# Kernel optimization log

Measured on AMD Instinct MI355X. Metric: run time of the kernel, lower is better.

Reference implementation:

```python
import jax, jax.numpy as jnp
import numpy as np

B, D, E, H = 8192, 512, 16, 128  # batch, input_dim, num_experts, hidden_dim
EPS = 1e-5  # BatchNorm eps (torch default)


def setup_inputs() -> dict:
    key = jax.random.key(0)
    ks = iter(jax.random.split(key, 32))
    def n(shape, s=0.05):
        return jax.random.normal(next(ks), shape, dtype=jnp.float32) * s
    inp = {"x": jax.random.normal(next(ks), (B, D), dtype=jnp.float32)}
    # Router params, stacked over the 2 branches (gender, race)
    inp["rbn_gamma"] = jnp.ones((2, D), jnp.float32)
    inp["rbn_beta"] = jnp.zeros((2, D), jnp.float32)
    inp["rbn_mean"] = n((2, D))
    inp["rbn_var"] = jnp.ones((2, D), jnp.float32)
    inp["rW1"], inp["rb1"] = n((2, D, 64)), jnp.full((2, 64), 0.1, jnp.float32)
    inp["rW2"], inp["rb2"] = n((2, 64, 32)), jnp.full((2, 32), 0.1, jnp.float32)
    inp["rW3"], inp["rb3"] = n((2, 32, E)), jnp.full((2, E), 0.1, jnp.float32)
    # Expert params, stacked over [branch=2, expert=16]
    inp["ebn_gamma"] = jnp.ones((2, E, D), jnp.float32)
    inp["ebn_beta"] = jnp.zeros((2, E, D), jnp.float32)
    inp["ebn_mean"] = n((2, E, D))
    inp["ebn_var"] = jnp.ones((2, E, D), jnp.float32)
    inp["eW1"], inp["eb1"] = n((2, E, D, H)), jnp.full((2, E, H), 0.1, jnp.float32)
    inp["eW2"], inp["eb2"] = n((2, E, H, H // 2)), jnp.full((2, E, H // 2), 0.1, jnp.float32)
    inp["eW3"], inp["eb3"] = n((2, E, H // 2)), jnp.full((2, E), 0.1, jnp.float32)
    inp["branch_weights"] = jnp.array([0.5, 0.5], jnp.float32)
    return inp


def reference(x, rbn_gamma, rbn_beta, rbn_mean, rbn_var, rW1, rb1, rW2, rb2,
              rW3, rb3, ebn_gamma, ebn_beta, ebn_mean, ebn_var, eW1, eb1,
              eW2, eb2, eW3, eb3, branch_weights):
    def branch(c):
        # Router: BN(eval) -> Linear(64) -> ReLU -> Linear(32) -> ReLU -> Linear(E) -> Softmax
        xn = (x - rbn_mean[c]) * jax.lax.rsqrt(rbn_var[c] + EPS) * rbn_gamma[c] + rbn_beta[c]
        h = jax.nn.relu(xn @ rW1[c] + rb1[c])
        h = jax.nn.relu(h @ rW2[c] + rb2[c])
        rw = jax.nn.softmax(h @ rW3[c] + rb3[c], axis=1)  # [B, E]
        # Experts batched over E: per-expert BN(eval) -> Linear -> ReLU -> Linear -> ReLU -> Linear -> sigmoid
        m, v = ebn_mean[c][:, None, :], ebn_var[c][:, None, :]
        g, b = ebn_gamma[c][:, None, :], ebn_beta[c][:, None, :]
        xe = (x[None] - m) * jax.lax.rsqrt(v + EPS) * g + b          # [E, B, D]
        h1 = jax.nn.relu(jnp.einsum('ebd,edh->ebh', xe, eW1[c]) + eb1[c][:, None, :])
        h2 = jax.nn.relu(jnp.einsum('ebh,ehk->ebk', h1, eW2[c]) + eb2[c][:, None, :])
        out = jax.nn.sigmoid(jnp.einsum('ebk,ek->eb', h2, eW3[c]) + eb3[c][:, None])  # [E, B]
        return jnp.einsum('be,eb->b', rw, out)                        # weighted sum over experts
    gender_pred = branch(0)
    race_pred = branch(1)
    return branch_weights[0] * gender_pred + branch_weights[1] * race_pred
```

## Files before the change

kernel.cpp:

```cpp
#include <hip/hip_runtime.h>

typedef __attribute__((ext_vector_type(8))) short short8;
typedef __attribute__((ext_vector_type(8))) unsigned short ushort8;
typedef __attribute__((ext_vector_type(4))) float f32x4;
typedef unsigned int u32;
typedef unsigned short u16;

#define AS_GLOBAL(p) ((const __attribute__((address_space(1))) u32*)(p))
#define AS_LDS(p) ((__attribute__((address_space(3))) u32*)(p))

#define NB 8192
#define ND 512
#define NH 128

#define OFF_XPK    0u
#define OFF_W1PK   8388608u
#define OFF_W2PK   12582912u
#define OFF_RW1PT  13107200u
#define OFF_B1P    13238272u
#define OFF_RB1P   13254656u
#define OFF_RWT    13255168u
#define OFF_PBIAS  14303744u

__device__ __forceinline__ u16 f2bf(float f) {
  union { float f; u32 u; } v; v.f = f;
  return (u16)((v.u + 0x7FFFu + ((v.u >> 16) & 1u)) >> 16);
}

__global__ __launch_bounds__(256) void k_prep_all(
    const float* __restrict__ x, u16* __restrict__ xpk,
    const float* __restrict__ eg, const float* __restrict__ ebb,
    const float* __restrict__ em, const float* __restrict__ ev,
    const float* __restrict__ eW1, u16* __restrict__ w1pk, float* __restrict__ pbias,
    const float* __restrict__ eW2, u16* __restrict__ w2pk,
    const float* __restrict__ rbn_g, const float* __restrict__ rbn_b,
    const float* __restrict__ rbn_m, const float* __restrict__ rbn_v,
    const float* __restrict__ rW1, const float* __restrict__ rb1,
    u16* __restrict__ rw1pt, float* __restrict__ rb1p,
    float* __restrict__ out)
{
  __shared__ __align__(16) unsigned char sh[17920];
  const int blk = blockIdx.x, t = threadIdx.x;
  if (blk < 2048) {
    int i = (blk * 256 + t) * 8;
    const float4* p = (const float4*)(x + i);
    float4 v0 = p[0], v1 = p[1];
    ushort8 r;
    r[0] = f2bf(v0.x); r[1] = f2bf(v0.y); r[2] = f2bf(v0.z); r[3] = f2bf(v0.w);
    r[4] = f2bf(v1.x); r[5] = f2bf(v1.y); r[6] = f2bf(v1.z); r[7] = f2bf(v1.w);
    int row = i >> 9, k0 = i & 511;
    int rb = row >> 4, lr = row & 15, kb = k0 >> 5, q = (k0 >> 3) & 3;
    *(ushort8*)(xpk + ((u32)(rb * 16 + kb) * 64 + q * 16 + lr) * 8) = r;
  } else if (blk < 2304) {
    float* sa = (float*)sh;
    float* sc = sa + 64;
    u16* tile = (u16*)(sc + 64);
    float* pb2 = (float*)(tile + 64 * 128);
    const int pair = (blk - 2048) >> 3, dc = (blk - 2048) & 7;
    const int d0 = dc * 64;
    if (t < 64) {
      int d = pair * ND + d0 + t;
      float a = eg[d] * rsqrtf(ev[d] + 1e-5f);
      sa[t] = a;
      sc[t] = ebb[d] - em[d] * a;
    }
    __syncthreads();
    const int h = t & 127, pr = t >> 7;
    float acc = 0.f;
    const float* src = eW1 + (size_t)pair * ND * NH + (size_t)d0 * NH;
#pragma unroll
    for (int i = 0; i < 32; ++i) {
      int dl = i * 2 + pr;
      float w = src[dl * NH + h];
      tile[dl * 128 + h] = f2bf(w * sa[dl]);
      acc += w * sc[dl];
    }
    pb2[pr * 128 + h] = acc;
    __syncthreads();
    {
      int hh = t >> 1, half = t & 1;
      const int nb = hh >> 4, lr = hh & 15;
#pragma unroll
      for (int v8 = 0; v8 < 4; ++v8) {
        int db = d0 + half * 32 + v8 * 8;
        int kb = db >> 5, q = (db >> 3) & 3;
        ushort8 r;
#pragma unroll
        for (int j = 0; j < 8; ++j) r[j] = tile[(half * 32 + v8 * 8 + j) * 128 + hh];
        *(ushort8*)(w1pk + (u32)((pair * 16 + kb) * 8 + nb) * 512 + (q * 16 + lr) * 8) = r;
      }
    }
    if (t < 128) pbias[(u32)(pair * 8 + dc) * 128 + t] = pb2[t] + pb2[128 + t];
  } else if (blk < 2336) {
    const int pair = blk - 2304;
    const float* w2 = eW2 + (size_t)pair * NH * 64;
    int n = t & 63, kk = t >> 6;
    for (int k = kk * 32; k < kk * 32 + 32; ++k) {
      u32 dst = ((u32)((pair * 4 + (k >> 5)) * 4 + (n >> 4))) * 512
              + (((k >> 3) & 3) * 16 + (n & 15)) * 8 + (k & 7);
      w2pk[dst] = f2bf(w2[k * 64 + n]);
    }
  } else if (blk < 2338) {
    const int c = blk - 2336;
    int n = t >> 2, q = t & 3;
    const float* g  = rbn_g + c * ND;
    const float* b  = rbn_b + c * ND;
    const float* m  = rbn_m + c * ND;
    const float* vv = rbn_v + c * ND;
    const float* w1 = rW1 + (size_t)c * ND * 64;
    float acc = 0.f;
    for (int d = q * 128; d < q * 128 + 128; ++d) {
      float a  = g[d] * rsqrtf(vv[d] + 1e-5f);
      float cc = b[d] - m[d] * a;
      float w  = w1[d * 64 + n];
      rw1pt[((u32)c * 64 + n) * ND + d] = f2bf(a * w);
      acc += cc * w;
    }
    acc += __shfl_xor(acc, 1, 64);
    acc += __shfl_xor(acc, 2, 64);
    if (q == 0) rb1p[c * 64 + n] = rb1[c * 64 + n] + acc;
  } else {
    float4 z; z.x = 0.f; z.y = 0.f; z.z = 0.f; z.w = 0.f;
    float4* o4 = (float4*)out;
#pragma unroll
    for (int j = 0; j < 8; ++j) o4[t * 8 + j] = z;
  }
}

__global__ __launch_bounds__(256) void k_router(
    const u16* __restrict__ xpk, const u16* __restrict__ rw1pt,
    const float* __restrict__ rb1p, const float* __restrict__ rW2,
    const float* __restrict__ rb2, const float* __restrict__ rW3,
    const float* __restrict__ rb3, float* __restrict__ rwT,
    const float* __restrict__ pbias, const float* __restrict__ eb1,
    float* __restrict__ b1p)
{
  __shared__ float h1l[64][65];
  __shared__ float h2l[64][33];
  __shared__ float w2s[2048];
  __shared__ float w3s[512];
  const int tid = threadIdx.x;
  if (blockIdx.x >= 256) {
    const int pair = blockIdx.x - 256;
    if (tid < 128) {
      float s = eb1[pair * NH + tid];
#pragma unroll
      for (int dc = 0; dc < 8; ++dc) s += pbias[(u32)(pair * 8 + dc) * 128 + tid];
      b1p[pair * NH + tid] = s;
    }
    return;
  }
  const int lane = tid & 63;
  const int wv = tid >> 6;
  const int q = lane >> 4;
  const int lr = lane & 15;
  const int c = blockIdx.x >> 7;
  const int r0 = (blockIdx.x & 127) * 64;

  {
    const float* W2 = rW2 + c * 2048;
    *(float4*)(w2s + tid * 8)     = *(const float4*)(W2 + tid * 8);
    *(float4*)(w2s + tid * 8 + 4) = *(const float4*)(W2 + tid * 8 + 4);
    if (tid < 128)
      *(float4*)(w3s + tid * 4) = *(const float4*)(rW3 + c * 512 + tid * 4);
  }

  f32x4 acc[4] = {};
  const u16* xfr   = xpk + ((u32)((r0 >> 4) + wv) * 16) * 512 + (u32)lane * 8;
  const u16* wbase = rw1pt + ((u32)c * 64 << 9);
  for (int kb = 0; kb < 16; ++kb) {
    short8 a = *(const short8*)(xfr + kb * 512);
#pragma unroll
    for (int u = 0; u < 4; ++u) {
      short8 b = *(const short8*)(wbase + (((u32)(u * 16 + lr)) << 9) + kb * 32 + q * 8);
      acc[u] = __builtin_amdgcn_mfma_f32_16x16x32_bf16(a, b, acc[u], 0, 0, 0);
    }
  }
#pragma unroll
  for (int u = 0; u < 4; ++u) {
    int n = u * 16 + lr;
    float bias = rb1p[c * 64 + n];
#pragma unroll
    for (int i = 0; i < 4; ++i) {
      float v = acc[u][i] + bias;
      h1l[wv * 16 + q * 4 + i][n] = v > 0.f ? v : 0.f;
    }
  }
  __syncthreads();
  {
    int row = tid >> 2, part = (tid & 3) * 8;
    float hv[8];
#pragma unroll
    for (int j = 0; j < 8; ++j) hv[j] = rb2[c * 32 + part + j];
#pragma unroll
    for (int k = 0; k < 64; ++k) {
      float hk = h1l[row][k];
#pragma unroll
      for (int j = 0; j < 8; ++j) hv[j] += hk * w2s[k * 32 + part + j];
    }
#pragma unroll
    for (int j = 0; j < 8; ++j) h2l[row][part + j] = hv[j] > 0.f ? hv[j] : 0.f;
  }
  __syncthreads();
  {
    int row = tid >> 2, e0 = (tid & 3) * 4;
    float lg[4];
#pragma unroll
    for (int e = 0; e < 4; ++e) {
      float a3 = rb3[c * 16 + e0 + e];
#pragma unroll
      for (int k = 0; k < 32; ++k) a3 += h2l[row][k] * w3s[k * 16 + e0 + e];
      lg[e] = a3;
    }
    float mx = fmaxf(fmaxf(lg[0], lg[1]), fmaxf(lg[2], lg[3]));
    mx = fmaxf(mx, __shfl_xor(mx, 1, 64));
    mx = fmaxf(mx, __shfl_xor(mx, 2, 64));
    float sm = 0.f;
#pragma unroll
    for (int e = 0; e < 4; ++e) { lg[e] = __expf(lg[e] - mx); sm += lg[e]; }
    sm += __shfl_xor(sm, 1, 64);
    sm += __shfl_xor(sm, 2, 64);
    float inv = 1.f / sm;
#pragma unroll
    for (int e = 0; e < 4; ++e)
      rwT[(u32)(c * 16 + e0 + e) * NB + r0 + row] = lg[e] * inv;
  }
}

__global__ __launch_bounds__(512, 2) void k_expert(
    const u16* __restrict__ xpk, const u16* __restrict__ w1pk,
    const float* __restrict__ b1p, const u16* __restrict__ w2pk,
    const float* __restrict__ eb2, const float* __restrict__ eW3,
    const float* __restrict__ eb3, const float* __restrict__ rwT,
    const float* __restrict__ bw, float* __restrict__ out)
{
  __shared__ __align__(16) unsigned char smem[65536];
  const int tid = threadIdx.x;
  const int lane = tid & 63;
  const int wv = tid >> 6;
  const int q = lane >> 4, lr = lane & 15;
  const int p = wv >> 2;
  const int wq = wv & 3;
  const int xcd  = blockIdx.x & 7;
  const int slot = blockIdx.x >> 3;
  const int pt   = xcd * 2 + (slot >> 5);
  const int bt   = slot & 31;
  const int pr0  = pt * 2;
  const int r0   = bt * 256;

  const u32 lane16 = (u32)lane * 16;

  const u16* stbase;
  u32 stlds, ststep, stjmul;
  if (wv < 4) {
    stbase = xpk + ((u32)(bt * 16 + wv * 4) * 16) * 512 + (u32)lane * 8;
    stlds  = (u32)wv * 4096;
    ststep = 512;
    stjmul = 8192;
  } else {
    const int g0 = (wv - 4) * 4;
    stbase = w1pk + ((u32)(pr0 + (g0 >> 3)) * 128 + (g0 & 7)) * 512 + (u32)lane * 8;
    stlds  = 16384 + (u32)(wv - 4) * 4096;
    ststep = 4096;
    stjmul = 512;
  }

#define STAGE(BUF, KB) do { \
  _Pragma("unroll") for (int j_ = 0; j_ < 4; ++j_) \
    __builtin_amdgcn_global_load_lds( \
        AS_GLOBAL(stbase + j_ * stjmul + (u32)(KB) * ststep), \
        AS_LDS(smem + (BUF) + stlds + j_ * 1024), 16, 0, 0); \
  } while (0)

  f32x4 acc[4][8] = {};

  STAGE(0, 0);
  STAGE(32768, 1);
  asm volatile("s_waitcnt vmcnt(4)" ::: "memory");
  __builtin_amdgcn_s_barrier();
  __builtin_amdgcn_sched_barrier(0);

#pragma unroll
  for (int kb = 0; kb < 16; ++kb) {
    const u32 BUF = (u32)(kb & 1) * 32768;
    short8 a_[4], b_[8];
#pragma unroll
    for (int t = 0; t < 4; ++t)
      a_[t] = *(const short8*)(smem + BUF + (u32)(wq * 4 + t) * 1024 + lane16);
#pragma unroll
    for (int u = 0; u < 8; ++u)
      b_[u] = *(const short8*)(smem + BUF + 16384 + (u32)(p * 8 + u) * 1024 + lane16);
    asm volatile("s_waitcnt lgkmcnt(0)" ::: "memory");
    __builtin_amdgcn_sched_barrier(0);
    if (kb < 14) {
      __builtin_amdgcn_s_barrier();
      __builtin_amdgcn_sched_barrier(0);
      STAGE(BUF, kb + 2);
      __builtin_amdgcn_sched_barrier(0);
    }
    __builtin_amdgcn_s_setprio(1);
#pragma unroll
    for (int t = 0; t < 4; ++t)
#pragma unroll
      for (int u = 0; u < 8; ++u)
        acc[t][u] = __builtin_amdgcn_mfma_f32_16x16x32_bf16(a_[t], b_[u], acc[t][u], 0, 0, 0);
    __builtin_amdgcn_s_setprio(0);
    __builtin_amdgcn_sched_barrier(0);
    if (kb < 14)       asm volatile("s_waitcnt vmcnt(4)" ::: "memory");
    else if (kb == 14) asm volatile("s_waitcnt vmcnt(0)" ::: "memory");
    if (kb < 15) {
      __builtin_amdgcn_s_barrier();
      __builtin_amdgcn_sched_barrier(0);
    }
  }
#undef STAGE

  __syncthreads();

#pragma unroll
  for (int pass = 0; pass < 2; ++pass) {
    const int pairG = pr0 + pass;
    if (p == pass) {
      float b1w[8];
#pragma unroll
      for (int u = 0; u < 8; ++u) b1w[u] = b1p[pairG * NH + u * 16 + lr];
#pragma unroll
      for (int t = 0; t < 4; ++t)
#pragma unroll
        for (int u = 0; u < 8; ++u) {
          const int rb = wq * 4 + t, kbh = u >> 1;
          const int qq = (u & 1) * 2 + (lr >> 3), jj = lr & 7;
#pragma unroll
          for (int i = 0; i < 4; ++i) {
            float v = acc[t][u][i] + b1w[u];
            v = v > 0.f ? v : 0.f;
            u32 byteoff = ((u32)((rb * 4 + kbh) * 64 + qq * 16 + q * 4 + i)) * 16 + jj * 2;
            *(u16*)(smem + byteoff) = f2bf(v);
          }
        }
    }
    __syncthreads();

    f32x4 acc2[2][4] = {};
#pragma unroll
    for (int kk = 0; kk < 4; ++kk) {
      short8 a2[2], b2[4];
#pragma unroll
      for (int t2 = 0; t2 < 2; ++t2)
        a2[t2] = *(const short8*)(smem + ((u32)((wv * 2 + t2) * 4 + kk)) * 1024 + lane16);
#pragma unroll
      for (int u2 = 0; u2 < 4; ++u2)
        b2[u2] = *(const short8*)(w2pk + ((u32)((pairG * 4 + kk) * 4 + u2)) * 512 + (u32)lane * 8);
#pragma unroll
      for (int t2 = 0; t2 < 2; ++t2)
#pragma unroll
        for (int u2 = 0; u2 < 4; ++u2)
          acc2[t2][u2] = __builtin_amdgcn_mfma_f32_16x16x32_bf16(a2[t2], b2[u2], acc2[t2][u2], 0, 0, 0);
    }

    {
      float bb2[4], bw3v[4];
#pragma unroll
      for (int u2 = 0; u2 < 4; ++u2) {
        bb2[u2]  = eb2[pairG * 64 + u2 * 16 + lr];
        bw3v[u2] = eW3[pairG * 64 + u2 * 16 + lr];
      }
      float b3 = eb3[pairG];
      float bwc = bw[pairG >> 4];
#pragma unroll
      for (int t2 = 0; t2 < 2; ++t2) {
        float pp[4] = {0.f, 0.f, 0.f, 0.f};
#pragma unroll
        for (int u2 = 0; u2 < 4; ++u2)
#pragma unroll
          for (int i = 0; i < 4; ++i) {
            float h = acc2[t2][u2][i] + bb2[u2];
            h = h > 0.f ? h : 0.f;
            pp[i] += h * bw3v[u2];
          }
#pragma unroll
        for (int m = 1; m < 16; m <<= 1)
#pragma unroll
          for (int i = 0; i < 4; ++i) pp[i] += __shfl_xor(pp[i], m, 64);
        if (lr == 0) {
#pragma unroll
          for (int i = 0; i < 4; ++i) {
            int row = wv * 32 + t2 * 16 + q * 4 + i;
            float z = pp[i] + b3;
            float s = 1.f / (1.f + __expf(-z));
            float rw = rwT[(u32)pairG * NB + r0 + row];
            atomicAdd(out + r0 + row, bwc * rw * s);
          }
        }
      }
    }
    __syncthreads();
  }
}

extern "C" void kernel_launch(void* const* d_in, const int* in_sizes, int n_in,
                              void* d_out, int out_size, void* d_ws, size_t ws_size,
                              hipStream_t stream) {
  const float* x     = (const float*)d_in[0];
  const float* rbn_g = (const float*)d_in[1];
  const float* rbn_b = (const float*)d_in[2];
  const float* rbn_m = (const float*)d_in[3];
  const float* rbn_v = (const float*)d_in[4];
  const float* rW1   = (const float*)d_in[5];
  const float* rb1   = (const float*)d_in[6];
  const float* rW2   = (const float*)d_in[7];
  const float* rb2   = (const float*)d_in[8];
  const float* rW3   = (const float*)d_in[9];
  const float* rb3   = (const float*)d_in[10];
  const float* ebn_g = (const float*)d_in[11];
  const float* ebn_b = (const float*)d_in[12];
  const float* ebn_m = (const float*)d_in[13];
  const float* ebn_v = (const float*)d_in[14];
  const float* eW1   = (const float*)d_in[15];
  const float* eb1   = (const float*)d_in[16];
  const float* eW2   = (const float*)d_in[17];
  const float* eb2   = (const float*)d_in[18];
  const float* eW3   = (const float*)d_in[19];
  const float* eb3   = (const float*)d_in[20];
  const float* bw    = (const float*)d_in[21];

  char* ws = (char*)d_ws;
  u16*   xpk   = (u16*)(ws + OFF_XPK);
  u16*   w1pk  = (u16*)(ws + OFF_W1PK);
  u16*   w2pk  = (u16*)(ws + OFF_W2PK);
  u16*   rw1pt = (u16*)(ws + OFF_RW1PT);
  float* b1p   = (float*)(ws + OFF_B1P);
  float* rb1p  = (float*)(ws + OFF_RB1P);
  float* rwT   = (float*)(ws + OFF_RWT);
  float* pbias = (float*)(ws + OFF_PBIAS);
  float* outf  = (float*)d_out;

  k_prep_all<<<dim3(2339), dim3(256), 0, stream>>>(
      x, xpk, ebn_g, ebn_b, ebn_m, ebn_v, eW1, w1pk, pbias, eW2, w2pk,
      rbn_g, rbn_b, rbn_m, rbn_v, rW1, rb1, rw1pt, rb1p, outf);
  k_router<<<dim3(288), dim3(256), 0, stream>>>(
      xpk, rw1pt, rb1p, rW2, rb2, rW3, rb3, rwT, pbias, eb1, b1p);
  k_expert<<<dim3(512), dim3(512), 0, stream>>>(
      xpk, w1pk, b1p, w2pk, eb2, eW3, eb3, rwT, bw, outf);
}
```

Measured before the change: 92.18 us.

## Fuse router into expert kernel, replace atomics with combine pass, interleave LDS loads

New measurement: 117.9 us. +27.9%, slower.

```diff
diff --git a/kernel.cpp b/kernel.cpp
--- a/kernel.cpp
+++ b/kernel.cpp
@@ -17,14 +17,18 @@
 #define OFF_W1PK   8388608u
 #define OFF_W2PK   12582912u
 #define OFF_RW1PT  13107200u
-#define OFF_B1P    13238272u
-#define OFF_RB1P   13254656u
-#define OFF_RWT    13255168u
-#define OFF_PBIAS  14303744u
+#define OFF_RB1P   13238272u
+#define OFF_PBIAS  13238784u
+#define OFF_RWT    13369856u
+#define OFF_ST     14418432u
 
 __device__ __forceinline__ u16 f2bf(float f) {
   union { float f; u32 u; } v; v.f = f;
   return (u16)((v.u + 0x7FFFu + ((v.u >> 16) & 1u)) >> 16);
+}
+__device__ __forceinline__ float bf2f(u16 h) {
+  union { u32 u; float f; } v; v.u = (u32)h << 16;
+  return v.f;
 }
 
 __global__ __launch_bounds__(256) void k_prep_all(
@@ -36,8 +40,7 @@
     const float* __restrict__ rbn_g, const float* __restrict__ rbn_b,
     const float* __restrict__ rbn_m, const float* __restrict__ rbn_v,
     const float* __restrict__ rW1, const float* __restrict__ rb1,
-    u16* __restrict__ rw1pt, float* __restrict__ rb1p,
-    float* __restrict__ out)
+    u16* __restrict__ rw1pt, float* __restrict__ rb1p)
 {
   __shared__ __align__(16) unsigned char sh[17920];
   const int blk = blockIdx.x, t = threadIdx.x;
@@ -100,7 +103,7 @@
               + (((k >> 3) & 3) * 16 + (n & 15)) * 8 + (k & 7);
       w2pk[dst] = f2bf(w2[k * 64 + n]);
     }
-  } else if (blk < 2338) {
+  } else {
     const int c = blk - 2336;
     int n = t >> 2, q = t & 3;
     const float* g  = rbn_g + c * ND;
@@ -119,123 +122,106 @@
     acc += __shfl_xor(acc, 1, 64);
     acc += __shfl_xor(acc, 2, 64);
     if (q == 0) rb1p[c * 64 + n] = rb1[c * 64 + n] + acc;
-  } else {
-    float4 z; z.x = 0.f; z.y = 0.f; z.z = 0.f; z.w = 0.f;
-    float4* o4 = (float4*)out;
-#pragma unroll
-    for (int j = 0; j < 8; ++j) o4[t * 8 + j] = z;
-  }
-}
-
-__global__ __launch_bounds__(256) void k_router(
-    const u16* __restrict__ xpk, const u16* __restrict__ rw1pt,
-    const float* __restrict__ rb1p, const float* __restrict__ rW2,
-    const float* __restrict__ rb2, const float* __restrict__ rW3,
-    const float* __restrict__ rb3, float* __restrict__ rwT,
+  }
+}
+
+__global__ __launch_bounds__(512) void k_fused(
+    const u16* __restrict__ xpk, const u16* __restrict__ w1pk,
     const float* __restrict__ pbias, const float* __restrict__ eb1,
-    float* __restrict__ b1p)
-{
-  __shared__ float h1l[64][65];
-  __shared__ float h2l[64][33];
-  __shared__ float w2s[2048];
-  __shared__ float w3s[512];
-  const int tid = threadIdx.x;
-  if (blockIdx.x >= 256) {
-    const int pair = blockIdx.x - 256;
-    if (tid < 128) {
-      float s = eb1[pair * NH + tid];
-#pragma unroll
-      for (int dc = 0; dc < 8; ++dc) s += pbias[(u32)(pair * 8 + dc) * 128 + tid];
-      b1p[pair * NH + tid] = s;
-    }
-    return;
-  }
-  const int lane = tid & 63;
-  const int wv = tid >> 6;
-  const int q = lane >> 4;
-  const int lr = lane & 15;
-  const int c = blockIdx.x >> 7;
-  const int r0 = (blockIdx.x & 127) * 64;
-
-  {
-    const float* W2 = rW2 + c * 2048;
-    *(float4*)(w2s + tid * 8)     = *(const float4*)(W2 + tid * 8);
-    *(float4*)(w2s + tid * 8 + 4) = *(const float4*)(W2 + tid * 8 + 4);
-    if (tid < 128)
-      *(float4*)(w3s + tid * 4) = *(const float4*)(rW3 + c * 512 + tid * 4);
-  }
-
-  f32x4 acc[4] = {};
-  const u16* xfr   = xpk + ((u32)((r0 >> 4) + wv) * 16) * 512 + (u32)lane * 8;
-  const u16* wbase = rw1pt + ((u32)c * 64 << 9);
-  for (int kb = 0; kb < 16; ++kb) {
-    short8 a = *(const short8*)(xfr + kb * 512);
-#pragma unroll
-    for (int u = 0; u < 4; ++u) {
-      short8 b = *(const short8*)(wbase + (((u32)(u * 16 + lr)) << 9) + kb * 32 + q * 8);
-      acc[u] = __builtin_amdgcn_mfma_f32_16x16x32_bf16(a, b, acc[u], 0, 0, 0);
-    }
-  }
-#pragma unroll
-  for (int u = 0; u < 4; ++u) {
-    int n = u * 16 + lr;
-    float bias = rb1p[c * 64 + n];
-#pragma unroll
-    for (int i = 0; i < 4; ++i) {
-      float v = acc[u][i] + bias;
-      h1l[wv * 16 + q * 4 + i][n] = v > 0.f ? v : 0.f;
-    }
-  }
-  __syncthreads();
-  {
-    int row = tid >> 2, part = (tid & 3) * 8;
-    float hv[8];
-#pragma unroll
-    for (int j = 0; j < 8; ++j) hv[j] = rb2[c * 32 + part + j];
-#pragma unroll
-    for (int k = 0; k < 64; ++k) {
-      float hk = h1l[row][k];
-#pragma unroll
-      for (int j = 0; j < 8; ++j) hv[j] += hk * w2s[k * 32 + part + j];
-    }
-#pragma unroll
-    for (int j = 0; j < 8; ++j) h2l[row][part + j] = hv[j] > 0.f ? hv[j] : 0.f;
-  }
-  __syncthreads();
-  {
-    int row = tid >> 2, e0 = (tid & 3) * 4;
-    float lg[4];
-#pragma unroll
-    for (int e = 0; e < 4; ++e) {
-      float a3 = rb3[c * 16 + e0 + e];
-#pragma unroll
-      for (int k = 0; k < 32; ++k) a3 += h2l[row][k] * w3s[k * 16 + e0 + e];
-      lg[e] = a3;
-    }
-    float mx = fmaxf(fmaxf(lg[0], lg[1]), fmaxf(lg[2], lg[3]));
-    mx = fmaxf(mx, __shfl_xor(mx, 1, 64));
-    mx = fmaxf(mx, __shfl_xor(mx, 2, 64));
-    float sm = 0.f;
-#pragma unroll
-    for (int e = 0; e < 4; ++e) { lg[e] = __expf(lg[e] - mx); sm += lg[e]; }
-    sm += __shfl_xor(sm, 1, 64);
-    sm += __shfl_xor(sm, 2, 64);
-    float inv = 1.f / sm;
-#pragma unroll
-    for (int e = 0; e < 4; ++e)
-      rwT[(u32)(c * 16 + e0 + e) * NB + r0 + row] = lg[e] * inv;
-  }
-}
-
-__global__ __launch_bounds__(512, 2) void k_expert(
-    const u16* __restrict__ xpk, const u16* __restrict__ w1pk,
-    const float* __restrict__ b1p, const u16* __restrict__ w2pk,
+    const u16* __restrict__ w2pk,
     const float* __restrict__ eb2, const float* __restrict__ eW3,
-    const float* __restrict__ eb3, const float* __restrict__ rwT,
-    const float* __restrict__ bw, float* __restrict__ out)
+    const float* __restrict__ eb3, u16* __restrict__ sT,
+    const u16* __restrict__ rw1pt, const float* __restrict__ rb1p,
+    const float* __restrict__ rW2, const float* __restrict__ rb2,
+    const float* __restrict__ rW3, const float* __restrict__ rb3,
+    float* __restrict__ rwT)
 {
   __shared__ __align__(16) unsigned char smem[65536];
   const int tid = threadIdx.x;
+
+  if (blockIdx.x >= 512) {
+    if (tid >= 256) return;
+    float* h1l = (float*)smem;
+    float* h2l = (float*)(smem + 16640);
+    float* w2s = (float*)(smem + 25088);
+    float* w3s = (float*)(smem + 33280);
+    const int idx = blockIdx.x - 512;
+    const int lane = tid & 63;
+    const int wv = tid >> 6;
+    const int q = lane >> 4;
+    const int lr = lane & 15;
+    const int c = idx >> 7;
+    const int r0 = (idx & 127) * 64;
+    {
+      const float* W2 = rW2 + c * 2048;
+      *(float4*)(w2s + tid * 8)     = *(const float4*)(W2 + tid * 8);
+      *(float4*)(w2s + tid * 8 + 4) = *(const float4*)(W2 + tid * 8 + 4);
+      if (tid < 128)
+        *(float4*)(w3s + tid * 4) = *(const float4*)(rW3 + c * 512 + tid * 4);
+    }
+    f32x4 acc[4] = {};
+    const u16* xfr   = xpk + ((u32)((r0 >> 4) + wv) * 16) * 512 + (u32)lane * 8;
+    const u16* wbase = rw1pt + ((u32)c * 64 << 9);
+    for (int kb = 0; kb < 16; ++kb) {
+      short8 a = *(const short8*)(xfr + kb * 512);
+#pragma unroll
+      for (int u = 0; u < 4; ++u) {
+        short8 b = *(const short8*)(wbase + (((u32)(u * 16 + lr)) << 9) + kb * 32 + q * 8);
+        acc[u] = __builtin_amdgcn_mfma_f32_16x16x32_bf16(a, b, acc[u], 0, 0, 0);
+      }
+    }
+#pragma unroll
+    for (int u = 0; u < 4; ++u) {
+      int n = u * 16 + lr;
+      float bias = rb1p[c * 64 + n];
+#pragma unroll
+      for (int i = 0; i < 4; ++i) {
+        float v = acc[u][i] + bias;
+        h1l[(wv * 16 + q * 4 + i) * 65 + n] = v > 0.f ? v : 0.f;
+      }
+    }
+    __syncthreads();
+    {
+      int row = tid >> 2, part = (tid & 3) * 8;
+      float hv[8];
+#pragma unroll
+      for (int j = 0; j < 8; ++j) hv[j] = rb2[c * 32 + part + j];
+#pragma unroll
+      for (int k = 0; k < 64; ++k) {
+        float hk = h1l[row * 65 + k];
+#pragma unroll
+        for (int j = 0; j < 8; ++j) hv[j] += hk * w2s[k * 32 + part + j];
+      }
+#pragma unroll
+      for (int j = 0; j < 8; ++j) h2l[row * 33 + part + j] = hv[j] > 0.f ? hv[j] : 0.f;
+    }
+    __syncthreads();
+    {
+      int row = tid >> 2, e0 = (tid & 3) * 4;
+      float lg[4];
+#pragma unroll
+      for (int e = 0; e < 4; ++e) {
+        float a3 = rb3[c * 16 + e0 + e];
+#pragma unroll
+        for (int k = 0; k < 32; ++k) a3 += h2l[row * 33 + k] * w3s[k * 16 + e0 + e];
+        lg[e] = a3;
+      }
+      float mx = fmaxf(fmaxf(lg[0], lg[1]), fmaxf(lg[2], lg[3]));
+      mx = fmaxf(mx, __shfl_xor(mx, 1, 64));
+      mx = fmaxf(mx, __shfl_xor(mx, 2, 64));
+      float sm = 0.f;
+#pragma unroll
+      for (int e = 0; e < 4; ++e) { lg[e] = __expf(lg[e] - mx); sm += lg[e]; }
+      sm += __shfl_xor(sm, 1, 64);
+      sm += __shfl_xor(sm, 2, 64);
+      float inv = 1.f / sm;
+#pragma unroll
+      for (int e = 0; e < 4; ++e)
+        rwT[(u32)(c * 16 + e0 + e) * NB + r0 + row] = lg[e] * inv;
+    }
+    return;
+  }
+
   const int lane = tid & 63;
   const int wv = tid >> 6;
   const int q = lane >> 4, lr = lane & 15;
@@ -247,7 +233,6 @@
   const int bt   = slot & 31;
   const int pr0  = pt * 2;
   const int r0   = bt * 256;
-
   const u32 lane16 = (u32)lane * 16;
 
   const u16* stbase;
@@ -271,6 +256,9 @@
         AS_GLOBAL(stbase + j_ * stjmul + (u32)(KB) * ststep), \
         AS_LDS(smem + (BUF) + stlds + j_ * 1024), 16, 0, 0); \
   } while (0)
+#define SB __builtin_amdgcn_sched_barrier(0)
+#define LDA(T) (*(const short8*)(smem + BUF + (u32)(wq * 4 + (T)) * 1024 + lane16))
+#define LDB(U) (*(const short8*)(smem + BUF + 16384 + (u32)(p * 8 + (U)) * 1024 + lane16))
 
   f32x4 acc[4][8] = {};
 
@@ -278,42 +266,65 @@
   STAGE(32768, 1);
   asm volatile("s_waitcnt vmcnt(4)" ::: "memory");
   __builtin_amdgcn_s_barrier();
-  __builtin_amdgcn_sched_barrier(0);
+  SB;
 
 #pragma unroll
   for (int kb = 0; kb < 16; ++kb) {
     const u32 BUF = (u32)(kb & 1) * 32768;
-    short8 a_[4], b_[8];
-#pragma unroll
-    for (int t = 0; t < 4; ++t)
-      a_[t] = *(const short8*)(smem + BUF + (u32)(wq * 4 + t) * 1024 + lane16);
-#pragma unroll
-    for (int u = 0; u < 8; ++u)
-      b_[u] = *(const short8*)(smem + BUF + 16384 + (u32)(p * 8 + u) * 1024 + lane16);
-    asm volatile("s_waitcnt lgkmcnt(0)" ::: "memory");
-    __builtin_amdgcn_sched_barrier(0);
+    short8 a_[4];
+    a_[0] = LDA(0); a_[1] = LDA(1); a_[2] = LDA(2); a_[3] = LDA(3);
+    short8 b_0 = LDB(0), b_1 = LDB(1);
+    short8 b_2 = LDB(2), b_3 = LDB(3);
+    SB; asm volatile("s_waitcnt lgkmcnt(2)" ::: "memory"); SB;
+    __builtin_amdgcn_s_setprio(1);
+#pragma unroll
+    for (int t = 0; t < 4; ++t) {
+      acc[t][0] = __builtin_amdgcn_mfma_f32_16x16x32_bf16(a_[t], b_0, acc[t][0], 0, 0, 0);
+      acc[t][1] = __builtin_amdgcn_mfma_f32_16x16x32_bf16(a_[t], b_1, acc[t][1], 0, 0, 0);
+    }
+    __builtin_amdgcn_s_setprio(0); SB;
+    short8 b_4 = LDB(4), b_5 = LDB(5);
+    SB; asm volatile("s_waitcnt lgkmcnt(2)" ::: "memory"); SB;
+    __builtin_amdgcn_s_setprio(1);
+#pragma unroll
+    for (int t = 0; t < 4; ++t) {
+      acc[t][2] = __builtin_amdgcn_mfma_f32_16x16x32_bf16(a_[t], b_2, acc[t][2], 0, 0, 0);
+      acc[t][3] = __builtin_amdgcn_mfma_f32_16x16x32_bf16(a_[t], b_3, acc[t][3], 0, 0, 0);
+    }
+    __builtin_amdgcn_s_setprio(0); SB;
+    short8 b_6 = LDB(6), b_7 = LDB(7);
+    SB; asm volatile("s_waitcnt lgkmcnt(2)" ::: "memory"); SB;
+    __builtin_amdgcn_s_setprio(1);
+#pragma unroll
+    for (int t = 0; t < 4; ++t) {
+      acc[t][4] = __builtin_amdgcn_mfma_f32_16x16x32_bf16(a_[t], b_4, acc[t][4], 0, 0, 0);
+      acc[t][5] = __builtin_amdgcn_mfma_f32_16x16x32_bf16(a_[t], b_5, acc[t][5], 0, 0, 0);
+    }
+    __builtin_amdgcn_s_setprio(0); SB;
+    asm volatile("s_waitcnt lgkmcnt(0)" ::: "memory"); SB;
     if (kb < 14) {
       __builtin_amdgcn_s_barrier();
-      __builtin_amdgcn_sched_barrier(0);
+      SB;
       STAGE(BUF, kb + 2);
-      __builtin_amdgcn_sched_barrier(0);
+      SB;
     }
     __builtin_amdgcn_s_setprio(1);
 #pragma unroll
-    for (int t = 0; t < 4; ++t)
-#pragma unroll
-      for (int u = 0; u < 8; ++u)
-        acc[t][u] = __builtin_amdgcn_mfma_f32_16x16x32_bf16(a_[t], b_[u], acc[t][u], 0, 0, 0);
-    __builtin_amdgcn_s_setprio(0);
-    __builtin_amdgcn_sched_barrier(0);
+    for (int t = 0; t < 4; ++t) {
+      acc[t][6] = __builtin_amdgcn_mfma_f32_16x16x32_bf16(a_[t], b_6, acc[t][6], 0, 0, 0);
+      acc[t][7] = __builtin_amdgcn_mfma_f32_16x16x32_bf16(a_[t], b_7, acc[t][7], 0, 0, 0);
+    }
+    __builtin_amdgcn_s_setprio(0); SB;
     if (kb < 14)       asm volatile("s_waitcnt vmcnt(4)" ::: "memory");
     else if (kb == 14) asm volatile("s_waitcnt vmcnt(0)" ::: "memory");
     if (kb < 15) {
       __builtin_amdgcn_s_barrier();
-      __builtin_amdgcn_sched_barrier(0);
+      SB;
     }
   }
 #undef STAGE
+#undef LDA
+#undef LDB
 
   __syncthreads();
 
@@ -323,7 +334,13 @@
     if (p == pass) {
       float b1w[8];
 #pragma unroll
-      for (int u = 0; u < 8; ++u) b1w[u] = b1p[pairG * NH + u * 16 + lr];
+      for (int u = 0; u < 8; ++u) {
+        int n = u * 16 + lr;
+        float s = eb1[pairG * NH + n];
+#pragma unroll
+        for (int dc = 0; dc < 8; ++dc) s += pbias[(u32)(pairG * 8 + dc) * 128 + n];
+        b1w[u] = s;
+      }
 #pragma unroll
       for (int t = 0; t < 4; ++t)
 #pragma unroll
@@ -334,8 +351,12 @@
           for (int i = 0; i < 4; ++i) {
             float v = acc[t][u][i] + b1w[u];
             v = v > 0.f ? v : 0.f;
-            u32 byteoff = ((u32)((rb * 4 + kbh) * 64 + qq * 16 + q * 4 + i)) * 16 + jj * 2;
-            *(u16*)(smem + byteoff) = f2bf(v);
+            u32 hv = f2bf(v);
+            u32 pv = (u32)__shfl_xor((int)hv, 1, 64);
+            if ((lane & 1) == 0) {
+              u32 byteoff = ((u32)((rb * 4 + kbh) * 64 + qq * 16 + q * 4 + i)) * 16 + jj * 2;
+              *(u32*)(smem + byteoff) = hv | (pv << 16);
+            }
           }
         }
     }
@@ -366,7 +387,6 @@
         bw3v[u2] = eW3[pairG * 64 + u2 * 16 + lr];
       }
       float b3 = eb3[pairG];
-      float bwc = bw[pairG >> 4];
 #pragma unroll
       for (int t2 = 0; t2 < 2; ++t2) {
         float pp[4] = {0.f, 0.f, 0.f, 0.f};
@@ -388,14 +408,29 @@
             int row = wv * 32 + t2 * 16 + q * 4 + i;
             float z = pp[i] + b3;
             float s = 1.f / (1.f + __expf(-z));
-            float rw = rwT[(u32)pairG * NB + r0 + row];
-            atomicAdd(out + r0 + row, bwc * rw * s);
+            sT[(u32)pairG * NB + r0 + row] = f2bf(s);
           }
         }
       }
     }
     __syncthreads();
   }
+#undef SB
+}
+
+__global__ __launch_bounds__(256) void k_combine(
+    const float* __restrict__ rwT, const u16* __restrict__ sT,
+    const float* __restrict__ bw, float* __restrict__ out)
+{
+  int b = blockIdx.x * 256 + threadIdx.x;
+  float bw0 = bw[0], bw1 = bw[1];
+  float acc0 = 0.f, acc1 = 0.f;
+#pragma unroll
+  for (int e = 0; e < 16; ++e) {
+    acc0 += rwT[(u32)e * NB + b] * bf2f(sT[(u32)e * NB + b]);
+    acc1 += rwT[(u32)(16 + e) * NB + b] * bf2f(sT[(u32)(16 + e) * NB + b]);
+  }
+  out[b] = bw0 * acc0 + bw1 * acc1;
 }
 
 extern "C" void kernel_launch(void* const* d_in, const int* in_sizes, int n_in,
@@ -429,17 +464,17 @@
   u16*   w1pk  = (u16*)(ws + OFF_W1PK);
   u16*   w2pk  = (u16*)(ws + OFF_W2PK);
   u16*   rw1pt = (u16*)(ws + OFF_RW1PT);
-  float* b1p   = (float*)(ws + OFF_B1P);
   float* rb1p  = (float*)(ws + OFF_RB1P);
+  float* pbias = (float*)(ws + OFF_PBIAS);
   float* rwT   = (float*)(ws + OFF_RWT);
-  float* pbias = (float*)(ws + OFF_PBIAS);
+  u16*   sT    = (u16*)(ws + OFF_ST);
   float* outf  = (float*)d_out;
 
-  k_prep_all<<<dim3(2339), dim3(256), 0, stream>>>(
+  k_prep_all<<<dim3(2338), dim3(256), 0, stream>>>(
       x, xpk, ebn_g, ebn_b, ebn_m, ebn_v, eW1, w1pk, pbias, eW2, w2pk,
-      rbn_g, rbn_b, rbn_m, rbn_v, rW1, rb1, rw1pt, rb1p, outf);
-  k_router<<<dim3(288), dim3(256), 0, stream>>>(
-      xpk, rw1pt, rb1p, rW2, rb2, rW3, rb3, rwT, pbias, eb1, b1p);
-  k_expert<<<dim3(512), dim3(512), 0, stream>>>(
-      xpk, w1pk, b1p, w2pk, eb2, eW3, eb3, rwT, bw, outf);
-}
+      rbn_g, rbn_b, rbn_m, rbn_v, rW1, rb1, rw1pt, rb1p);
+  k_fused<<<dim3(768), dim3(512), 0, stream>>>(
+      xpk, w1pk, pbias, eb1, w2pk, eb2, eW3, eb3, sT,
+      rw1pt, rb1p, rW2, rb2, rW3, rb3, rwT);
+  k_combine<<<dim3(NB / 256), dim3(256), 0, stream>>>(rwT, sT, bw, outf);
+}
```
